# Performance work log

Hardware: AMD Instinct MI355X
Metric: run time of the kernel (lower is better)

Reference implementation:

```python
import jax, jax.numpy as jnp
import numpy as np

DIM = 768
NUM_HEADS = 12
HEAD_DIM = DIM // NUM_HEADS
SCALE = HEAD_DIM ** -0.5
B, N = 4, 2048


def setup_inputs() -> dict:
    key = jax.random.key(0)
    k1, k2, k3 = jax.random.split(key, 3)
    x = jax.random.normal(k1, (B, N, DIM), dtype=jnp.float32)
    W_qk = jax.random.normal(k2, (2 * DIM, DIM), dtype=jnp.float32) * (DIM ** -0.5)
    b_qk = jax.random.normal(k3, (2 * DIM,), dtype=jnp.float32) * 0.02
    return {"x": x, "W_qk": W_qk, "b_qk": b_qk}


def reference(x, W_qk, b_qk):
    Bb, Nn, C = x.shape
    # qk projection: [B,N,2C] -> [B,N,2,H,D] -> q,k each [B,H,N,D]
    qk = x @ W_qk.T + b_qk
    qk = qk.reshape(Bb, Nn, 2, NUM_HEADS, HEAD_DIM).transpose(2, 0, 3, 1, 4)
    q, k = qk[0], qk[1]
    # attention scores [B,H,N,N]
    attn = jnp.einsum("bhnd,bhmd->bhnm", q, k) * SCALE
    attn = jax.nn.softmax(attn, axis=-1)
    # mean over heads, then per-query diagonal -> [B,N]
    attn_weights = jnp.diagonal(attn.mean(axis=1), axis1=-2, axis2=-1)
    return attn_weights
```

## Files before the change

### kernel.cpp

```cpp
#include <hip/hip_runtime.h>
#include <math.h>


#define B_ 4
#define N_ 2048
#define H_ 12
#define D_ 64
#define C_ 768
#define TWO_C 1536
#define QSCALE 0.18033688011112043f

typedef _Float16 half8 __attribute__((ext_vector_type(8)));
typedef _Float16 half4 __attribute__((ext_vector_type(4)));
typedef float floatx4 __attribute__((ext_vector_type(4)));

#if __has_builtin(__builtin_amdgcn_exp2f)
#define EXP2(x) __builtin_amdgcn_exp2f(x)
#else
#define EXP2(x) exp2f(x)
#endif

__device__ __forceinline__ void gload_lds16(const _Float16* g, _Float16* l) {
  __builtin_amdgcn_global_load_lds(
      (const __attribute__((address_space(1))) void*)g,
      (__attribute__((address_space(3))) void*)l, 16, 0, 0);
}

#define NX4 1572864
#define NW4 294912
__global__ __launch_bounds__(256) void conv_kernel(const float* __restrict__ x,
                                                   const float* __restrict__ W,
                                                   _Float16* __restrict__ xh,
                                                   _Float16* __restrict__ wh) {
  int i = blockIdx.x * 256 + threadIdx.x;
  const float* in;
  _Float16* out;
  int idx;
  if (i < NX4) {
    in = x; out = xh; idx = i;
  } else if (i < NX4 + NW4) {
    in = W; out = wh; idx = i - NX4;
  } else {
    return;
  }
  float4 v = ((const float4*)in)[idx];
  half4 o;
  o[0] = (_Float16)v.x; o[1] = (_Float16)v.y;
  o[2] = (_Float16)v.z; o[3] = (_Float16)v.w;
  ((half4*)out)[idx] = o;
}

__global__ __launch_bounds__(256) void proj_kernel(
    const _Float16* __restrict__ xh, const _Float16* __restrict__ wh,
    const float* __restrict__ bias, _Float16* __restrict__ qh,
    _Float16* __restrict__ kh) {
  __shared__ _Float16 As[3][128 * 32];
  __shared__ _Float16 Bs[3][128 * 32];
  const int t = threadIdx.x;
  const int l = t & 63;
  const int w = t >> 6;
  const int wr = w >> 1, wc = w & 1;

  int lin = blockIdx.y * 12 + blockIdx.x;
  int swz = (lin & 7) * 96 + (lin >> 3);
  const int bm = (swz / 12) * 128;
  const int bc = (swz % 12) * 128;

  const int srow = l >> 2;
  const int schunk = (l & 3) ^ ((l >> 3) & 3);

  floatx4 acc[4][4] = {};

#define PSTAGE(KT)                                                          \
  {                                                                         \
    const int sl_ = (KT) % 3;                                               \
    const int k0_ = (KT) * 32;                                              \
    _Pragma("unroll") for (int i_ = 0; i_ < 2; ++i_) {                      \
      int rb_ = w * 32 + i_ * 16;                                           \
      gload_lds16(xh + (size_t)(bm + rb_ + srow) * C_ + k0_ + schunk * 8,   \
                  As[sl_] + rb_ * 32);                                      \
      gload_lds16(wh + (size_t)(bc + rb_ + srow) * C_ + k0_ + schunk * 8,   \
                  Bs[sl_] + rb_ * 32);                                      \
    }                                                                       \
  }

#define PITER(KT, VMASM, DO_STAGE)                                          \
  {                                                                         \
    asm volatile(VMASM ::: "memory");                                       \
    __builtin_amdgcn_s_barrier();                                           \
    asm volatile("" ::: "memory");                                          \
    const int sl_ = (KT) % 3;                                               \
    const _Float16* Ap_ = As[sl_];                                          \
    const _Float16* Bp_ = Bs[sl_];                                          \
    half8 af[4], bf[4];                                                     \
    _Pragma("unroll") for (int fr = 0; fr < 4; ++fr) {                      \
      int row = wr * 64 + fr * 16 + (l & 15);                               \
      int ch = (l >> 4) ^ ((row >> 1) & 3);                                 \
      af[fr] = *(const half8*)(Ap_ + row * 32 + ch * 8);                    \
    }                                                                       \
    _Pragma("unroll") for (int fc = 0; fc < 4; ++fc) {                      \
      int row = wc * 64 + fc * 16 + (l & 15);                               \
      int ch = (l >> 4) ^ ((row >> 1) & 3);                                 \
      bf[fc] = *(const half8*)(Bp_ + row * 32 + ch * 8);                    \
    }                                                                       \
    if (DO_STAGE) PSTAGE((KT) + 2);                                         \
    _Pragma("unroll") for (int fr = 0; fr < 4; ++fr)                        \
        _Pragma("unroll") for (int fc = 0; fc < 4; ++fc) acc[fr][fc] =      \
        __builtin_amdgcn_mfma_f32_16x16x32_f16(af[fr], bf[fc],              \
                                               acc[fr][fc], 0, 0, 0);       \
  }

  PSTAGE(0);
  PSTAGE(1);
  for (int kt = 0; kt < 22; ++kt) PITER(kt, "s_waitcnt vmcnt(4)", true);
  PITER(22, "s_waitcnt vmcnt(4)", false);
  PITER(23, "s_waitcnt vmcnt(0)", false);
#undef PITER
#undef PSTAGE

#pragma unroll
  for (int fr = 0; fr < 4; ++fr) {
#pragma unroll
    for (int fc = 0; fc < 4; ++fc) {
#pragma unroll
      for (int j = 0; j < 4; ++j) {
        int m = bm + wr * 64 + fr * 16 + ((l >> 4) << 2) + j;
        int c = bc + wc * 64 + fc * 16 + (l & 15);
        float v = acc[fr][fc][j] + bias[c];
        int b = m >> 11, n = m & (N_ - 1);
        int cc = (c < C_) ? c : c - C_;
        if (c < C_) v *= QSCALE;
        int hh = cc >> 6, d = cc & 63;
        _Float16* dst = (c < C_) ? qh : kh;
        dst[((((size_t)b * H_ + hh) * N_ + n) << 6) + d] = (_Float16)v;
      }
    }
  }
}

__global__ __launch_bounds__(256) void attn_kernel(
    const _Float16* __restrict__ qh, const _Float16* __restrict__ kh,
    float* __restrict__ part) {
  __shared__ _Float16 ks[4][4][1024];
  const int t = threadIdx.x;
  const int l = t & 63;
  const int w = t >> 6;

  int lin = blockIdx.x;
  int swz = (lin & 7) * 192 + (lin >> 3);
  const int qt = swz & 31;
  const int h = (swz >> 5) % 12;
  const int b = swz / 384;

  const _Float16* qb = qh + (((size_t)(b * H_ + h) * N_ + qt * 64) << 6);
  const _Float16* kb = kh + (((size_t)(b * H_ + h) * N_) << 6);

  half8 qf[4][2];
#pragma unroll
  for (int fr = 0; fr < 4; ++fr)
#pragma unroll
    for (int kd = 0; kd < 2; ++kd)
      qf[fr][kd] = *(const half8*)(qb + (size_t)(fr * 16 + (l & 15)) * 64 +
                                   kd * 32 + (l >> 4) * 8);

  const _Float16* ksrc = kb + (w * 16 + (l & 15)) * 64 + (l >> 4) * 8;

#define STAGE(KT)                                                   \
  {                                                                 \
    const _Float16* kp_ = ksrc + (size_t)(KT) * 4096;               \
    _Float16* ld_ = &ks[w][(KT) & 3][0];                            \
    gload_lds16(kp_, ld_);                                          \
    gload_lds16(kp_ + 32, ld_ + 512);                               \
  }

  float lsum[4][4] = {};
  float ed[4] = {0.f, 0.f, 0.f, 0.f};

  STAGE(0);
  STAGE(1);
  STAGE(2);

#define ITER(KT, VMASM, DO_STAGE)                                             \
  {                                                                           \
    asm volatile(VMASM ::: "memory");                                         \
    const _Float16* bufp = &ks[w][(KT) & 3][0];                               \
    half8 kf0 = *(const half8*)(bufp + l * 8);                                \
    half8 kf1 = *(const half8*)(bufp + 512 + l * 8);                          \
    if (DO_STAGE) STAGE((KT) + 3);                                            \
    floatx4 acc[4] = {};                                                      \
    _Pragma("unroll") for (int fr = 0; fr < 4; ++fr) {                        \
      acc[fr] = __builtin_amdgcn_mfma_f32_16x16x32_f16(qf[fr][0], kf0,        \
                                                       acc[fr], 0, 0, 0);     \
      acc[fr] = __builtin_amdgcn_mfma_f32_16x16x32_f16(qf[fr][1], kf1,        \
                                                       acc[fr], 0, 0, 0);     \
    }                                                                         \
    _Pragma("unroll") for (int fr = 0; fr < 4; ++fr)                          \
        _Pragma("unroll") for (int j = 0; j < 4; ++j) {                       \
      float e = EXP2(acc[fr][j]);                                             \
      lsum[fr][j] += e;                                                       \
    }                                                                         \
    if ((KT) == qt) {                                                         \
      _Pragma("unroll") for (int fr = 0; fr < 4; ++fr)                        \
          _Pragma("unroll") for (int j = 0; j < 4; ++j) {                     \
        if (fr == w && (l & 15) == (((l >> 4) << 2) + j))                     \
          ed[j] = EXP2(acc[fr][j]);                                           \
      }                                                                       \
    }                                                                         \
  }

  for (int kt = 0; kt < 29; ++kt) ITER(kt, "s_waitcnt vmcnt(4)", true);
  ITER(29, "s_waitcnt vmcnt(4)", false);
  ITER(30, "s_waitcnt vmcnt(2)", false);
  ITER(31, "s_waitcnt vmcnt(0)", false);
#undef ITER
#undef STAGE

#pragma unroll
  for (int fr = 0; fr < 4; ++fr)
#pragma unroll
    for (int j = 0; j < 4; ++j)
#pragma unroll
      for (int m = 1; m < 16; m <<= 1)
        lsum[fr][j] += __shfl_xor(lsum[fr][j], m, 16);
#pragma unroll
  for (int j = 0; j < 4; ++j)
#pragma unroll
    for (int m = 1; m < 16; m <<= 1) ed[j] += __shfl_xor(ed[j], m, 16);

  __syncthreads();
  float* red = (float*)&ks[0][0][0];
  float* edl = red + 256;
  if ((l & 15) == 0) {
#pragma unroll
    for (int fr = 0; fr < 4; ++fr)
#pragma unroll
      for (int j = 0; j < 4; ++j)
        red[w * 64 + fr * 16 + ((l >> 4) << 2) + j] = lsum[fr][j];
#pragma unroll
    for (int j = 0; j < 4; ++j) edl[w * 16 + ((l >> 4) << 2) + j] = ed[j];
  }
  __syncthreads();

  if (t < 64) {
    float ls = red[t] + red[64 + t] + red[128 + t] + red[192 + t];
    part[(size_t)(b * H_ + h) * N_ + qt * 64 + t] = edl[t] / ls;
  }
}

__global__ __launch_bounds__(256) void reduce_kernel(
    const float* __restrict__ part, float* __restrict__ out) {
  int g = blockIdx.x * 256 + threadIdx.x;
  if (g >= B_ * N_) return;
  int b = g >> 11, n = g & (N_ - 1);
  float s = 0.0f;
#pragma unroll
  for (int hh = 0; hh < H_; ++hh) s += part[(size_t)(b * H_ + hh) * N_ + n];
  out[g] = s * (1.0f / (float)H_);
}

extern "C" void kernel_launch(void* const* d_in, const int* in_sizes, int n_in,
                              void* d_out, int out_size, void* d_ws,
                              size_t ws_size, hipStream_t stream) {
  const float* x = (const float*)d_in[0];
  const float* W = (const float*)d_in[1];
  const float* bias = (const float*)d_in[2];
  float* out = (float*)d_out;

  char* ws = (char*)d_ws;
  _Float16* xh = (_Float16*)ws;
  _Float16* wh = (_Float16*)(ws + 12582912);
  _Float16* qh = (_Float16*)(ws + 14942208);
  _Float16* kh = (_Float16*)(ws + 27525120);
  float* part = (float*)(ws + 40108032);

  conv_kernel<<<(NX4 + NW4 + 255) / 256, 256, 0, stream>>>(x, W, xh, wh);
  proj_kernel<<<dim3(TWO_C / 128, 8192 / 128), 256, 0, stream>>>(xh, wh, bias,
                                                                 qh, kh);
  attn_kernel<<<N_ / 64 * H_ * B_, 256, 0, stream>>>(qh, kh, part);
  reduce_kernel<<<(B_ * N_ + 255) / 256, 256, 0, stream>>>(part, out);
}
```

Baseline: 93.43 us.

## Share swizzled K tiles across waves and software-pipeline exp with MFMA

Each wave previously loaded its own 16-row slice of K into a private LDS buffer. Now all four waves cooperatively load a full 64x64 K tile into shared LDS with an XOR swizzle to avoid bank conflicts, and each wave reads its rows back. The exp2/sum of the previous tile is interleaved with the MFMAs of the current tile using two ping-ponged accumulator sets. This adds a workgroup barrier every iteration, which may stall waves.

```diff
diff --git a/kernel.cpp b/kernel.cpp
--- a/kernel.cpp
+++ b/kernel.cpp
@@ -141,7 +141,7 @@
 __global__ __launch_bounds__(256) void attn_kernel(
     const _Float16* __restrict__ qh, const _Float16* __restrict__ kh,
     float* __restrict__ part) {
-  __shared__ _Float16 ks[4][4][1024];
+  __shared__ _Float16 ks[4][64 * 64];
   const int t = threadIdx.x;
   const int l = t & 63;
   const int w = t >> 6;
@@ -163,56 +163,78 @@
       qf[fr][kd] = *(const half8*)(qb + (size_t)(fr * 16 + (l & 15)) * 64 +
                                    kd * 32 + (l >> 4) * 8);
 
-  const _Float16* ksrc = kb + (w * 16 + (l & 15)) * 64 + (l >> 4) * 8;
+  const int lin0 = w * 64 + l;
+  const int row0 = lin0 >> 3, slot0 = lin0 & 7;
+  const int soff0 = row0 * 64 + (slot0 ^ (row0 & 7)) * 8;
+  const int lin1 = lin0 + 256;
+  const int row1 = lin1 >> 3, slot1 = lin1 & 7;
+  const int soff1 = row1 * 64 + (slot1 ^ (row1 & 7)) * 8;
 
 #define STAGE(KT)                                                   \
   {                                                                 \
-    const _Float16* kp_ = ksrc + (size_t)(KT) * 4096;               \
-    _Float16* ld_ = &ks[w][(KT) & 3][0];                            \
-    gload_lds16(kp_, ld_);                                          \
-    gload_lds16(kp_ + 32, ld_ + 512);                               \
-  }
+    const _Float16* kp_ = kb + (size_t)(KT) * 4096;                 \
+    _Float16* ld_ = ks[(KT) & 3];                                   \
+    gload_lds16(kp_ + soff0, ld_ + w * 512);                        \
+    gload_lds16(kp_ + soff1, ld_ + w * 512 + 2048);                 \
+  }
+
+  const int frow = w * 16 + (l & 15);
+  const int koff0 = frow * 64 + (((l >> 4) + 0) ^ (l & 7)) * 8;
+  const int koff1 = frow * 64 + (((l >> 4) + 4) ^ (l & 7)) * 8;
 
   float lsum[4][4] = {};
   float ed[4] = {0.f, 0.f, 0.f, 0.f};
-
-  STAGE(0);
-  STAGE(1);
-  STAGE(2);
-
-#define ITER(KT, VMASM, DO_STAGE)                                             \
+  const floatx4 kZero = {0.f, 0.f, 0.f, 0.f};
+  floatx4 accA[4], accB[4];
+
+#define FINB(KT, ACC)                                                         \
   {                                                                           \
-    asm volatile(VMASM ::: "memory");                                         \
-    const _Float16* bufp = &ks[w][(KT) & 3][0];                               \
-    half8 kf0 = *(const half8*)(bufp + l * 8);                                \
-    half8 kf1 = *(const half8*)(bufp + 512 + l * 8);                          \
-    if (DO_STAGE) STAGE((KT) + 3);                                            \
-    floatx4 acc[4] = {};                                                      \
-    _Pragma("unroll") for (int fr = 0; fr < 4; ++fr) {                        \
-      acc[fr] = __builtin_amdgcn_mfma_f32_16x16x32_f16(qf[fr][0], kf0,        \
-                                                       acc[fr], 0, 0, 0);     \
-      acc[fr] = __builtin_amdgcn_mfma_f32_16x16x32_f16(qf[fr][1], kf1,        \
-                                                       acc[fr], 0, 0, 0);     \
-    }                                                                         \
     _Pragma("unroll") for (int fr = 0; fr < 4; ++fr)                          \
-        _Pragma("unroll") for (int j = 0; j < 4; ++j) {                       \
-      float e = EXP2(acc[fr][j]);                                             \
-      lsum[fr][j] += e;                                                       \
-    }                                                                         \
+        _Pragma("unroll") for (int j = 0; j < 4; ++j)                         \
+            lsum[fr][j] += EXP2(ACC[fr][j]);                                  \
     if ((KT) == qt) {                                                         \
       _Pragma("unroll") for (int fr = 0; fr < 4; ++fr)                        \
           _Pragma("unroll") for (int j = 0; j < 4; ++j) {                     \
         if (fr == w && (l & 15) == (((l >> 4) << 2) + j))                     \
-          ed[j] = EXP2(acc[fr][j]);                                           \
+          ed[j] = EXP2(ACC[fr][j]);                                           \
       }                                                                       \
     }                                                                         \
   }
 
-  for (int kt = 0; kt < 29; ++kt) ITER(kt, "s_waitcnt vmcnt(4)", true);
-  ITER(29, "s_waitcnt vmcnt(4)", false);
-  ITER(30, "s_waitcnt vmcnt(2)", false);
-  ITER(31, "s_waitcnt vmcnt(0)", false);
-#undef ITER
+#define STEP(KT, ACCC, ACCP, VMASM, DO_STAGE, DO_FIN)                         \
+  {                                                                           \
+    asm volatile(VMASM ::: "memory");                                         \
+    __builtin_amdgcn_s_barrier();                                             \
+    asm volatile("" ::: "memory");                                            \
+    const _Float16* bufp = ks[(KT) & 3];                                      \
+    half8 kf0 = *(const half8*)(bufp + koff0);                                \
+    half8 kf1 = *(const half8*)(bufp + koff1);                                \
+    if (DO_STAGE) STAGE((KT) + 3);                                            \
+    if (DO_FIN) FINB((KT) - 1, ACCP);                                         \
+    _Pragma("unroll") for (int fr = 0; fr < 4; ++fr) {                        \
+      ACCC[fr] = kZero;                                                       \
+      ACCC[fr] = __builtin_amdgcn_mfma_f32_16x16x32_f16(qf[fr][0], kf0,       \
+                                                        ACCC[fr], 0, 0, 0);   \
+      ACCC[fr] = __builtin_amdgcn_mfma_f32_16x16x32_f16(qf[fr][1], kf1,       \
+                                                        ACCC[fr], 0, 0, 0);   \
+    }                                                                         \
+  }
+
+  STAGE(0);
+  STAGE(1);
+  STAGE(2);
+
+  STEP(0, accA, accB, "s_waitcnt vmcnt(4)", true, false);
+  for (int kt = 1; kt < 28; kt += 2) {
+    STEP(kt, accB, accA, "s_waitcnt vmcnt(4)", true, true);
+    STEP(kt + 1, accA, accB, "s_waitcnt vmcnt(4)", true, true);
+  }
+  STEP(29, accB, accA, "s_waitcnt vmcnt(4)", false, true);
+  STEP(30, accA, accB, "s_waitcnt vmcnt(2)", false, true);
+  STEP(31, accB, accA, "s_waitcnt vmcnt(0)", false, true);
+  FINB(31, accB);
+#undef STEP
+#undef FINB
 #undef STAGE
 
 #pragma unroll
@@ -227,8 +249,8 @@
 #pragma unroll
     for (int m = 1; m < 16; m <<= 1) ed[j] += __shfl_xor(ed[j], m, 16);
 
-  __syncthreads();
-  float* red = (float*)&ks[0][0][0];
+  __builtin_amdgcn_s_barrier();
+  float* red = (float*)ks[0];
   float* edl = red + 256;
   if ((l & 15) == 0) {
 #pragma unroll
```

Result: faster. 84.45 us (-9.6%).

## Share K tiles across waves with swizzled LDS and fold head reduction into atomics

Applied to the files above, without the earlier changes.

The attention kernel now loads each 64-row K tile into LDS once per block. It uses an XOR-swizzled layout to avoid bank conflicts, and all four waves read fragments from it behind a per-iteration barrier, where previously each wave staged only its own slice. The separate reduce kernel is removed: the output is zeroed in the conversion kernel and each attention block atomically adds its per-head contribution scaled by 1/H. This trades a kernel launch and a partial-result buffer for atomics and an extra barrier per K step. The sum accumulation is also vectorised.

```diff
diff --git a/kernel.cpp b/kernel.cpp
--- a/kernel.cpp
+++ b/kernel.cpp
@@ -31,8 +31,13 @@
 __global__ __launch_bounds__(256) void conv_kernel(const float* __restrict__ x,
                                                    const float* __restrict__ W,
                                                    _Float16* __restrict__ xh,
-                                                   _Float16* __restrict__ wh) {
+                                                   _Float16* __restrict__ wh,
+                                                   float* __restrict__ outz) {
   int i = blockIdx.x * 256 + threadIdx.x;
+  if (i < 2048) {
+    float4 z; z.x = 0.f; z.y = 0.f; z.z = 0.f; z.w = 0.f;
+    ((float4*)outz)[i] = z;
+  }
   const float* in;
   _Float16* out;
   int idx;
@@ -140,8 +145,8 @@
 
 __global__ __launch_bounds__(256) void attn_kernel(
     const _Float16* __restrict__ qh, const _Float16* __restrict__ kh,
-    float* __restrict__ part) {
-  __shared__ _Float16 ks[4][4][1024];
+    float* __restrict__ out) {
+  __shared__ _Float16 ks[4][64 * 64];
   const int t = threadIdx.x;
   const int l = t & 63;
   const int w = t >> 6;
@@ -163,17 +168,26 @@
       qf[fr][kd] = *(const half8*)(qb + (size_t)(fr * 16 + (l & 15)) * 64 +
                                    kd * 32 + (l >> 4) * 8);
 
-  const _Float16* ksrc = kb + (w * 16 + (l & 15)) * 64 + (l >> 4) * 8;
+  const int lin0 = w * 64 + l;
+  const int row0 = lin0 >> 3, slot0 = lin0 & 7;
+  const int soff0 = row0 * 64 + (slot0 ^ (row0 & 7)) * 8;
+  const int lin1 = lin0 + 256;
+  const int row1 = lin1 >> 3, slot1 = lin1 & 7;
+  const int soff1 = row1 * 64 + (slot1 ^ (row1 & 7)) * 8;
 
 #define STAGE(KT)                                                   \
   {                                                                 \
-    const _Float16* kp_ = ksrc + (size_t)(KT) * 4096;               \
-    _Float16* ld_ = &ks[w][(KT) & 3][0];                            \
-    gload_lds16(kp_, ld_);                                          \
-    gload_lds16(kp_ + 32, ld_ + 512);                               \
-  }
-
-  float lsum[4][4] = {};
+    const _Float16* kp_ = kb + (size_t)(KT) * 4096;                 \
+    _Float16* ld_ = ks[(KT) & 3];                                   \
+    gload_lds16(kp_ + soff0, ld_ + w * 512);                        \
+    gload_lds16(kp_ + soff1, ld_ + w * 512 + 2048);                 \
+  }
+
+  const int frow = w * 16 + (l & 15);
+  const int koff0 = frow * 64 + (((l >> 4) + 0) ^ (l & 7)) * 8;
+  const int koff1 = frow * 64 + (((l >> 4) + 4) ^ (l & 7)) * 8;
+
+  floatx4 lsum[4] = {};
   float ed[4] = {0.f, 0.f, 0.f, 0.f};
 
   STAGE(0);
@@ -183,9 +197,11 @@
 #define ITER(KT, VMASM, DO_STAGE)                                             \
   {                                                                           \
     asm volatile(VMASM ::: "memory");                                         \
-    const _Float16* bufp = &ks[w][(KT) & 3][0];                               \
-    half8 kf0 = *(const half8*)(bufp + l * 8);                                \
-    half8 kf1 = *(const half8*)(bufp + 512 + l * 8);                          \
+    __builtin_amdgcn_s_barrier();                                             \
+    asm volatile("" ::: "memory");                                            \
+    const _Float16* bufp = ks[(KT) & 3];                                      \
+    half8 kf0 = *(const half8*)(bufp + koff0);                                \
+    half8 kf1 = *(const half8*)(bufp + koff1);                                \
     if (DO_STAGE) STAGE((KT) + 3);                                            \
     floatx4 acc[4] = {};                                                      \
     _Pragma("unroll") for (int fr = 0; fr < 4; ++fr) {                        \
@@ -194,10 +210,10 @@
       acc[fr] = __builtin_amdgcn_mfma_f32_16x16x32_f16(qf[fr][1], kf1,        \
                                                        acc[fr], 0, 0, 0);     \
     }                                                                         \
-    _Pragma("unroll") for (int fr = 0; fr < 4; ++fr)                          \
-        _Pragma("unroll") for (int j = 0; j < 4; ++j) {                       \
-      float e = EXP2(acc[fr][j]);                                             \
-      lsum[fr][j] += e;                                                       \
+    _Pragma("unroll") for (int fr = 0; fr < 4; ++fr) {                        \
+      floatx4 ev;                                                             \
+      _Pragma("unroll") for (int j = 0; j < 4; ++j) ev[j] = EXP2(acc[fr][j]); \
+      lsum[fr] += ev;                          \
     }                                                                         \
     if ((KT) == qt) {                                                         \
       _Pragma("unroll") for (int fr = 0; fr < 4; ++fr)                        \
@@ -227,8 +243,8 @@
 #pragma unroll
     for (int m = 1; m < 16; m <<= 1) ed[j] += __shfl_xor(ed[j], m, 16);
 
-  __syncthreads();
-  float* red = (float*)&ks[0][0][0];
+  __builtin_amdgcn_s_barrier();
+  float* red = (float*)ks[0];
   float* edl = red + 256;
   if ((l & 15) == 0) {
 #pragma unroll
@@ -243,19 +259,9 @@
 
   if (t < 64) {
     float ls = red[t] + red[64 + t] + red[128 + t] + red[192 + t];
-    part[(size_t)(b * H_ + h) * N_ + qt * 64 + t] = edl[t] / ls;
-  }
-}
-
-__global__ __launch_bounds__(256) void reduce_kernel(
-    const float* __restrict__ part, float* __restrict__ out) {
-  int g = blockIdx.x * 256 + threadIdx.x;
-  if (g >= B_ * N_) return;
-  int b = g >> 11, n = g & (N_ - 1);
-  float s = 0.0f;
-#pragma unroll
-  for (int hh = 0; hh < H_; ++hh) s += part[(size_t)(b * H_ + hh) * N_ + n];
-  out[g] = s * (1.0f / (float)H_);
+    atomicAdd(out + (size_t)b * N_ + qt * 64 + t,
+              edl[t] / ls * (1.0f / (float)H_));
+  }
 }
 
 extern "C" void kernel_launch(void* const* d_in, const int* in_sizes, int n_in,
@@ -271,11 +277,9 @@
   _Float16* wh = (_Float16*)(ws + 12582912);
   _Float16* qh = (_Float16*)(ws + 14942208);
   _Float16* kh = (_Float16*)(ws + 27525120);
-  float* part = (float*)(ws + 40108032);
-
-  conv_kernel<<<(NX4 + NW4 + 255) / 256, 256, 0, stream>>>(x, W, xh, wh);
+
+  conv_kernel<<<(NX4 + NW4 + 255) / 256, 256, 0, stream>>>(x, W, xh, wh, out);
   proj_kernel<<<dim3(TWO_C / 128, 8192 / 128), 256, 0, stream>>>(xh, wh, bias,
                                                                  qh, kh);
-  attn_kernel<<<N_ / 64 * H_ * B_, 256, 0, stream>>>(qh, kh, part);
-  reduce_kernel<<<(B_ * N_ + 255) / 256, 256, 0, stream>>>(part, out);
-}
+  attn_kernel<<<N_ / 64 * H_ * B_, 256, 0, stream>>>(qh, kh, out);
+}
```

Measured after the change: 81.70 us. 12.6% less time.
